# Kernel tuning notes

Measured on AMD Instinct MI355X. Metric: run time of the kernel, lower is better.

The kernel has to match this reference:

```python
import jax, jax.numpy as jnp
import numpy as np
from jax import lax

N_FRAMES = 256

def _conv(x, w, b):
    # NCHW conv, stride 3 on mel axis (matches MOSNet CNN that collapses mels 81->27->9->3->1)
    y = lax.conv_general_dilated(x, w, window_strides=(1, 3),
                                 padding=((1, 1), (1, 1)),
                                 dimension_numbers=('NCHW', 'OIHW', 'NCHW'))
    return jax.nn.relu(y + b[None, :, None, None])

def _lstm(x, Wih, Whh, bih, bhh, reverse=False):
    # x: [T, B, D] -> hs: [T, B, H]; PyTorch gate order i, f, g, o
    Bsz, H = x.shape[1], Whh.shape[1]
    bias = bih + bhh
    def step(carry, xt):
        h, c = carry
        z = xt @ Wih.T + h @ Whh.T + bias
        i, f, g, o = jnp.split(z, 4, axis=-1)
        c = jax.nn.sigmoid(f) * c + jax.nn.sigmoid(i) * jnp.tanh(g)
        h = jax.nn.sigmoid(o) * jnp.tanh(c)
        return (h, c), h
    init = (jnp.zeros((Bsz, H), x.dtype), jnp.zeros((Bsz, H), x.dtype))
    _, hs = lax.scan(step, init, x, reverse=reverse)
    return hs

def setup_inputs():
    key = jax.random.key(0)
    ks = jax.random.split(key, 24)
    B, T, M = 16, 4096, 81
    chans = [1, 16, 32, 64, 128]
    H = 128
    FC_IN = 2 * H * N_FRAMES  # 65536
    FC_H = 128
    s = 0.05
    inp = {'audio': jax.random.normal(ks[0], (B, T, M), jnp.float32),
           'sample_lengths': jnp.full((B,), T, dtype=jnp.int32)}
    for li in range(4):
        inp['w%d' % li] = jax.random.normal(ks[1 + 2 * li], (chans[li + 1], chans[li], 3, 3), jnp.float32) * s
        inp['b%d' % li] = jnp.zeros((chans[li + 1],), jnp.float32)
    D = chans[-1]
    for d, off in (('f', 9), ('b', 13)):
        inp['Wih_' + d] = jax.random.normal(ks[off], (4 * H, D), jnp.float32) * s
        inp['Whh_' + d] = jax.random.normal(ks[off + 1], (4 * H, H), jnp.float32) * s
        inp['bih_' + d] = jnp.zeros((4 * H,), jnp.float32)
        inp['bhh_' + d] = jnp.zeros((4 * H,), jnp.float32)
    inp['fc1_w'] = jax.random.normal(ks[17], (FC_H, FC_IN), jnp.float32) * 0.005
    inp['fc1_b'] = jnp.zeros((FC_H,), jnp.float32)
    inp['fs_w'] = jax.random.normal(ks[18], (1, FC_H), jnp.float32) * s
    inp['fs_b'] = jnp.zeros((1,), jnp.float32)
    return inp

def reference(audio, w0, b0, w1, b1, w2, b2, w3, b3,
              Wih_f, Whh_f, bih_f, bhh_f, Wih_b, Whh_b, bih_b, bhh_b,
              fc1_w, fc1_b, fs_w, fs_b, sample_lengths):
    B, T, M = audio.shape
    F = T // N_FRAMES  # all lengths == T, multiple of N_FRAMES -> all frames full
    x = audio.reshape(B * F, 1, N_FRAMES, M)   # [BF, 1, nf, mels]
    for w, b in ((w0, b0), (w1, b1), (w2, b2), (w3, b3)):
        x = _conv(x, w, b)                      # mel axis 81->27->9->3->1
    x = x[..., 0].transpose(2, 0, 1)            # [nf, BF, C]
    h_f = _lstm(x, Wih_f, Whh_f, bih_f, bhh_f)
    h_b = _lstm(x, Wih_b, Whh_b, bih_b, bhh_b, reverse=True)
    h = jnp.concatenate([h_f, h_b], axis=-1).transpose(1, 0, 2)  # [BF, nf, 2H]
    flat = h.reshape(B * F, -1)                 # time-major flatten, matches view(1,-1)
    z = jax.nn.relu(flat @ fc1_w.T + fc1_b)     # dropout is identity at inference
    score = jax.nn.sigmoid(z @ fs_w.T + fs_b) * 4.0 + 1.0  # mos range [1,5]
    frames = score.reshape(B, F)
    utt = frames.mean(axis=1)
    return utt, frames
```

## Files before the change

### kernel.cpp

```cpp
#include <hip/hip_runtime.h>
#include <hip/hip_fp16.h>

#define BF 256
#define TSTEPS 256

typedef _Float16 h8_t __attribute__((ext_vector_type(8)));
typedef _Float16 h4_t __attribute__((ext_vector_type(4)));
typedef float f4_t __attribute__((ext_vector_type(4)));

union H8 { uint4 u; h8_t v; };
union H4 { uint2 u; h4_t v; };
union U2H4 { uint2 u; __half h[4]; };

static __device__ __forceinline__ float sigmoidf_(float x) {
    return __builtin_amdgcn_rcpf(1.f + __expf(-x));
}
static __device__ __forceinline__ float tanhf_(float x) {
    return 1.f - 2.f * __builtin_amdgcn_rcpf(__expf(2.f * x) + 1.f);
}

static __device__ __forceinline__ void wg_barrier_lds() {
    __builtin_amdgcn_sched_barrier(0);
    asm volatile("s_waitcnt lgkmcnt(0)" ::: "memory");
    __builtin_amdgcn_s_barrier();
    __builtin_amdgcn_sched_barrier(0);
}

static __device__ __forceinline__ void pack_one(const float* __restrict__ src,
                                                __half* __restrict__ dst,
                                                int OC, int IC, int KS,
                                                int oc_str, int ic_str, int k_str, int i) {
    int grp = KS / 4;
    int j = i % grp;
    int oc = (i / grp) % OC;
    int g = (i / (grp * OC)) & 3;
    int chunk = i / (grp * OC * 4);
    int CPK = IC / KS;
    int cc = chunk % CPK;
    int khw = chunk / CPK;
    int ic = cc * KS + g * grp + j;
    dst[i] = __float2half(src[(long)oc * oc_str + (long)ic * ic_str + khw * k_str]);
}

static __device__ __forceinline__ void pack_whh_one(const float* __restrict__ src,
                                                    __half* __restrict__ dst, int i) {
    int j = i & 7;
    int prow = (i >> 3) & 511;
    int cg = i >> 12;
    int g = cg & 3, chunk = cg >> 2;
    int t = prow >> 4, rr = prow & 15;
    int cls = rr >> 2, du = rr & 3;
    int orig = cls * 128 + t * 4 + du;
    int ic = chunk * 32 + g * 8 + j;
    dst[i] = __float2half(src[orig * 128 + ic]);
}

__global__ __launch_bounds__(256) void prep_k(
        const float* __restrict__ w0, const float* __restrict__ w1,
        const float* __restrict__ w2, const float* __restrict__ w3,
        const float* __restrict__ Wihf, const float* __restrict__ Wihb,
        const float* __restrict__ Whhf, const float* __restrict__ Whhb,
        float* __restrict__ w0t, __half* __restrict__ w1p,
        __half* __restrict__ w2p, __half* __restrict__ w3p,
        __half* __restrict__ wfp, __half* __restrict__ wbp,
        __half* __restrict__ whhfp, __half* __restrict__ whhbp) {
    int i = blockIdx.x * 256 + threadIdx.x;
    if (i < 144) { int oc = i / 9, rem = i % 9; w0t[rem * 16 + oc] = w0[i]; return; }
    i -= 144;
    if (i < 4608) { pack_one(w1, w1p, 32, 16, 16, 144, 9, 1, i); return; }
    i -= 4608;
    if (i < 18432) { pack_one(w2, w2p, 64, 32, 32, 288, 9, 1, i); return; }
    i -= 18432;
    if (i < 73728) { pack_one(w3, w3p, 128, 64, 32, 576, 9, 1, i); return; }
    i -= 73728;
    if (i < 65536) { pack_one(Wihf, wfp, 512, 128, 32, 128, 1, 0, i); return; }
    i -= 65536;
    if (i < 65536) { pack_one(Wihb, wbp, 512, 128, 32, 128, 1, 0, i); return; }
    i -= 65536;
    if (i < 65536) { pack_whh_one(Whhf, whhfp, i); return; }
    i -= 65536;
    if (i < 65536) { pack_whh_one(Whhb, whhbp, i); return; }
}

__global__ void pack_wf16(const float* __restrict__ src, __half* __restrict__ dst,
                          int OC, int IC, int KS,
                          int oc_str, int ic_str, int k_str, int total) {
    int i = blockIdx.x * 256 + threadIdx.x;
    if (i >= total) return;
    pack_one(src, dst, OC, IC, KS, oc_str, ic_str, k_str, i);
}

__global__ __launch_bounds__(256) void conv0_k(const float* __restrict__ in,
                                               const float* __restrict__ wT,
                                               const float* __restrict__ bias,
                                               __half* __restrict__ out) {
    __shared__ float wsm[9][16];
    __shared__ float bs[16];
    int tid = threadIdx.x;
    if (tid < 144) wsm[tid / 16][tid % 16] = wT[tid];
    if (tid < 16) bs[tid] = bias[tid];
    __syncthreads();
    int gid = blockIdx.x * 256 + tid;
    int ow = gid % 27;
    int t = (gid / 27) % 256;
    int bf = gid / (27 * 256);
    float acc[16];
#pragma unroll
    for (int o = 0; o < 16; o++) acc[o] = bs[o];
    int iw0 = ow * 3 - 1;
#pragma unroll
    for (int kh = 0; kh < 3; kh++) {
        int tt = t + kh - 1;
        if ((unsigned)tt >= 256u) continue;
        const float* ip = in + ((long)bf * 256 + tt) * 81;
#pragma unroll
        for (int kw = 0; kw < 3; kw++) {
            int iw = iw0 + kw;
            if ((unsigned)iw >= 81u) continue;
            float x = ip[iw];
#pragma unroll
            for (int o = 0; o < 16; o++) acc[o] += x * wsm[kh * 3 + kw][o];
        }
    }
    __half2* op = (__half2*)(out + (long)gid * 16);
#pragma unroll
    for (int o = 0; o < 8; o++)
        op[o] = __floats2half2_rn(fmaxf(acc[2 * o], 0.f), fmaxf(acc[2 * o + 1], 0.f));
}

template<int IC, int OC, int WIN, int WOUT, int KS>
__global__ __launch_bounds__(256) void convM_k(const __half* __restrict__ in,
                                               const __half* __restrict__ wp,
                                               const float* __restrict__ bias,
                                               __half* __restrict__ out) {
    constexpr int NT = OC / 16;
    constexpr int CPK = IC / KS;
    constexpr int NCHUNK = 9 * CPK;
    constexpr int GRP = KS / 4;
    int tid = threadIdx.x;
    int lane = tid & 63;
    int wv = tid >> 6;
    int l15 = lane & 15;
    int g = lane >> 4;
    int m = blockIdx.x * 64 + wv * 16 + l15;
    int ow = m % WOUT;
    int t = (m / WOUT) % 256;
    int bf = m / (WOUT * 256);

    f4_t acc[NT];
#pragma unroll
    for (int nt = 0; nt < NT; nt++)
#pragma unroll
        for (int r = 0; r < 4; r++) acc[nt][r] = 0.f;

#pragma unroll
    for (int chunk = 0; chunk < NCHUNK; chunk++) {
        int khw = chunk / CPK, cc = chunk % CPK;
        int kh = khw / 3;
        int kw = khw - kh * 3;
        int tt = t + kh - 1;
        int iw = ow * 3 + kw - 1;
        bool ok = ((unsigned)tt < 256u) && ((unsigned)iw < (unsigned)WIN);
        long aoff = ok ? (((long)(bf * 256 + tt) * WIN + iw) * IC + cc * KS + g * GRP) : 0;
        if constexpr (KS == 32) {
            H8 af;
            af.u = *(const uint4*)(in + aoff);
            if (!ok) af.u = make_uint4(0u, 0u, 0u, 0u);
#pragma unroll
            for (int nt = 0; nt < NT; nt++) {
                H8 bf8;
                bf8.u = *(const uint4*)(wp + ((long)(chunk * 4 + g) * OC + nt * 16 + l15) * GRP);
                acc[nt] = __builtin_amdgcn_mfma_f32_16x16x32_f16(af.v, bf8.v, acc[nt], 0, 0, 0);
            }
        } else {
            H4 af;
            af.u = *(const uint2*)(in + aoff);
            if (!ok) af.u = make_uint2(0u, 0u);
#pragma unroll
            for (int nt = 0; nt < NT; nt++) {
                H4 bf4;
                bf4.u = *(const uint2*)(wp + ((long)(chunk * 4 + g) * OC + nt * 16 + l15) * GRP);
                acc[nt] = __builtin_amdgcn_mfma_f32_16x16x16f16(af.v, bf4.v, acc[nt], 0, 0, 0);
            }
        }
    }
    int orow = blockIdx.x * 64 + wv * 16 + g * 4;
#pragma unroll
    for (int nt = 0; nt < NT; nt++) {
        int oc = nt * 16 + l15;
        float b = bias[oc];
#pragma unroll
        for (int r = 0; r < 4; r++) {
            float v = fmaxf(acc[nt][r] + b, 0.f);
            out[(long)(orow + r) * OC + oc] = __float2half(v);
        }
    }
}

__global__ __launch_bounds__(256) void gates_k(const __half* __restrict__ X,
                                               const __half* __restrict__ wpf,
                                               const __half* __restrict__ wpb,
                                               const float* __restrict__ bf1,
                                               const float* __restrict__ bf2,
                                               const float* __restrict__ bb1,
                                               const float* __restrict__ bb2,
                                               __half* __restrict__ Gf,
                                               __half* __restrict__ Gb) {
    int dir = blockIdx.z;
    const __half* wp = dir ? wpb : wpf;
    const float* b1 = dir ? bb1 : bf1;
    const float* b2 = dir ? bb2 : bf2;
    __half* G = dir ? Gb : Gf;
    int tid = threadIdx.x;
    int lane = tid & 63;
    int wv = tid >> 6;
    int l15 = lane & 15;
    int g = lane >> 4;
    long r0 = (long)blockIdx.x * 128 + wv * 32;
    int n0 = blockIdx.y * 128;

    f4_t acc[2][8];
#pragma unroll
    for (int s = 0; s < 2; s++)
#pragma unroll
        for (int nt = 0; nt < 8; nt++)
#pragma unroll
            for (int r = 0; r < 4; r++) acc[s][nt][r] = 0.f;

#pragma unroll
    for (int chunk = 0; chunk < 4; chunk++) {
        H8 a0, a1;
        a0.u = *(const uint4*)(X + (r0 + l15) * 128 + chunk * 32 + g * 8);
        a1.u = *(const uint4*)(X + (r0 + 16 + l15) * 128 + chunk * 32 + g * 8);
#pragma unroll
        for (int nt = 0; nt < 8; nt++) {
            H8 bw;
            bw.u = *(const uint4*)(wp + ((long)(chunk * 4 + g) * 512 + n0 + nt * 16 + l15) * 8);
            acc[0][nt] = __builtin_amdgcn_mfma_f32_16x16x32_f16(a0.v, bw.v, acc[0][nt], 0, 0, 0);
            acc[1][nt] = __builtin_amdgcn_mfma_f32_16x16x32_f16(a1.v, bw.v, acc[1][nt], 0, 0, 0);
        }
    }
    int b = (int)(r0 >> 8);
#pragma unroll
    for (int nt = 0; nt < 8; nt++) {
        int col = n0 + nt * 16 + l15;
        float bias = b1[col] + b2[col];
        long base = ((long)b * 512 + col) * 256;
#pragma unroll
        for (int s = 0; s < 2; s++) {
            int tb = (int)(r0 & 255) + s * 16 + g * 4;
            U2H4 pk;
            if (!dir) {
#pragma unroll
                for (int r = 0; r < 4; r++) pk.h[r] = __float2half(acc[s][nt][r] + bias);
                *(uint2*)(G + base + tb) = pk.u;
            } else {
#pragma unroll
                for (int r = 0; r < 4; r++) pk.h[3 - r] = __float2half(acc[s][nt][r] + bias);
                *(uint2*)(G + base + (252 - tb)) = pk.u;
            }
        }
    }
}

__global__ __launch_bounds__(1024, 4) void lstm_k(const __half* __restrict__ Gf,
                                                  const __half* __restrict__ Gb,
                                                  const __half* __restrict__ whhfp,
                                                  const __half* __restrict__ whhbp,
                                                  __half* __restrict__ flat) {
    int bid = blockIdx.x;
    int dir = bid >> 7;
    int b0 = (bid & 127) * 2;
    const __half* G = dir ? Gb : Gf;
    const __half* wp = dir ? whhbp : whhfp;
    int tid = threadIdx.x;
    int w = tid >> 6;
    int lane = tid & 63;
    int l15 = lane & 15;
    int g2 = lane >> 4;
    int chn = l15 >> 3;
    int u8 = l15 & 7;
    int unit = w * 8 + u8;
    int tsel = (u8 >> 2) & 1;
    int du = u8 & 3;

    H8 afr[2][4];
#pragma unroll
    for (int t = 0; t < 2; t++) {
        int prow = (w * 2 + t) * 16 + l15;
#pragma unroll
        for (int c = 0; c < 4; c++)
            afr[t][c].u = *(const uint4*)(wp + ((long)((c * 4 + g2) * 512 + prow)) * 8);
    }

    __shared__ __align__(16) __half hbuf[2][2][128];
    if (tid < 256) hbuf[0][tid >> 7][tid & 127] = __float2half(0.f);
    __syncthreads();

    const __half* gb0 = G + (((long)(b0 + chn) * 512) + g2 * 128 + unit) * 256;

    float cst = 0.f;
    float ma = (g2 == 2) ? 2.f : 1.f;
    float mb = ma;
    float cb = (g2 == 2) ? -1.f : 0.f;
    const f4_t zero4 = {0.f, 0.f, 0.f, 0.f};

    H8 gc, gn;
    gc.u = *(const uint4*)(gb0);
    long fbase = (long)(b0 + chn) * 65536 + dir * 128 + unit;

    for (int to = 0; to < 32; to++) {
        if (to < 31) gn.u = *(const uint4*)(gb0 + (to + 1) * 8);
#pragma unroll
        for (int ti = 0; ti < 8; ti++) {
            int s = to * 8 + ti;
            int p = s & 1;
            H8 bfr[4];
#pragma unroll
            for (int c = 0; c < 4; c++)
                bfr[c].u = *(const uint4*)(&hbuf[p][chn][c * 32 + g2 * 8]);

            f4_t acc[2];
#pragma unroll
            for (int t = 0; t < 2; t++)
                acc[t] = __builtin_amdgcn_mfma_f32_16x16x32_f16(afr[t][0].v, bfr[0].v,
                                                                zero4, 0, 0, 0);
#pragma unroll
            for (int c = 1; c < 4; c++)
#pragma unroll
                for (int t = 0; t < 2; t++)
                    acc[t] = __builtin_amdgcn_mfma_f32_16x16x32_f16(afr[t][c].v, bfr[c].v,
                                                                    acc[t], 0, 0, 0);
            f4_t at;
#pragma unroll
            for (int e = 0; e < 4; e++) at[e] = tsel ? acc[1][e] : acc[0][e];
            float lo = (du & 1) ? at[1] : at[0];
            float hi = (du & 1) ? at[3] : at[2];
            float ev = (du & 2) ? hi : lo;

            float z = ev + (float)gc.v[ti];
            float a = sigmoidf_(ma * z) * mb + cb;

            float x1 = __shfl_xor(a, 32, 64);
            float pi = a * x1;
            float x2 = __shfl_xor(pi, 16, 64);
            float cn = a * cst + x2;
            cst = cn;
            float tc = tanhf_(cn);
            float x3 = __shfl_xor(tc, 32, 64);
            float h = a * x3;

            if (g2 == 3) {
                __half hh = __float2half(h);
                int ts = dir ? (255 - s) : s;
                hbuf[p ^ 1][chn][unit] = hh;
                flat[fbase + (long)ts * 256] = hh;
            }
            wg_barrier_lds();
        }
        gc = gn;
    }
}

__global__ __launch_bounds__(256) void fc1m_k(const __half* __restrict__ flat,
                                              const __half* __restrict__ wp,
                                              float* __restrict__ z) {
    int tid = threadIdx.x;
    int lane = tid & 63;
    int wv = tid >> 6;
    int l15 = lane & 15;
    int g = lane >> 4;
    int m0 = blockIdx.x * 64 + wv * 16;
    long k0 = (long)blockIdx.y * 1024;

    f4_t acc[8];
#pragma unroll
    for (int nt = 0; nt < 8; nt++)
#pragma unroll
        for (int r = 0; r < 4; r++) acc[nt][r] = 0.f;

    for (int c = 0; c < 32; c++) {
        long chunk = (k0 >> 5) + c;
        H8 af;
        af.u = *(const uint4*)(flat + (long)(m0 + l15) * 65536 + k0 + c * 32 + g * 8);
#pragma unroll
        for (int nt = 0; nt < 8; nt++) {
            H8 bw;
            bw.u = *(const uint4*)(wp + ((chunk * 4 + g) * 128 + nt * 16 + l15) * 8);
            acc[nt] = __builtin_amdgcn_mfma_f32_16x16x32_f16(af.v, bw.v, acc[nt], 0, 0, 0);
        }
    }
#pragma unroll
    for (int nt = 0; nt < 8; nt++)
#pragma unroll
        for (int r = 0; r < 4; r++)
            atomicAdd(&z[(m0 + g * 4 + r) * 128 + nt * 16 + l15], acc[nt][r]);
}

__global__ void zero_k(float* __restrict__ p, int n) {
    int i = blockIdx.x * 256 + threadIdx.x;
    if (i < n) p[i] = 0.f;
}

__global__ __launch_bounds__(256) void head_k(const float* __restrict__ z,
                                              const float* __restrict__ b1,
                                              const float* __restrict__ fsw,
                                              const float* __restrict__ fsb,
                                              float* __restrict__ out) {
    __shared__ float sf[256];
    int r = threadIdx.x;
    float acc = fsb[0];
#pragma unroll
    for (int j4 = 0; j4 < 32; j4++) {
        float4 zv = *(const float4*)&z[r * 128 + j4 * 4];
        float4 bv = *(const float4*)&b1[j4 * 4];
        float4 wv = *(const float4*)&fsw[j4 * 4];
        acc += fmaxf(zv.x + bv.x, 0.f) * wv.x;
        acc += fmaxf(zv.y + bv.y, 0.f) * wv.y;
        acc += fmaxf(zv.z + bv.z, 0.f) * wv.z;
        acc += fmaxf(zv.w + bv.w, 0.f) * wv.w;
    }
    float val = sigmoidf_(acc) * 4.f + 1.f;
    out[16 + r] = val;
    sf[r] = val;
    __syncthreads();
    if (r < 16) {
        float m = 0.f;
#pragma unroll
        for (int f = 0; f < 16; f++) m += sf[r * 16 + f];
        out[r] = m * (1.f / 16.f);
    }
}

extern "C" void kernel_launch(void* const* d_in, const int* in_sizes, int n_in,
                              void* d_out, int out_size, void* d_ws, size_t ws_size,
                              hipStream_t stream) {
    const float* audio = (const float*)d_in[0];
    const float* w0 = (const float*)d_in[2];
    const float* b0 = (const float*)d_in[3];
    const float* w1 = (const float*)d_in[4];
    const float* b1 = (const float*)d_in[5];
    const float* w2 = (const float*)d_in[6];
    const float* b2 = (const float*)d_in[7];
    const float* w3 = (const float*)d_in[8];
    const float* b3 = (const float*)d_in[9];
    const float* Wih_f = (const float*)d_in[10];
    const float* Whh_f = (const float*)d_in[11];
    const float* bih_f = (const float*)d_in[12];
    const float* bhh_f = (const float*)d_in[13];
    const float* Wih_b = (const float*)d_in[14];
    const float* Whh_b = (const float*)d_in[15];
    const float* bih_b = (const float*)d_in[16];
    const float* bhh_b = (const float*)d_in[17];
    const float* fc1_w = (const float*)d_in[18];
    const float* fc1_b = (const float*)d_in[19];
    const float* fs_w = (const float*)d_in[20];
    const float* fs_b = (const float*)d_in[21];
    float* out = (float*)d_out;

    char* ws = (char*)d_ws;
    __half* Gf    = (__half*)(ws);
    __half* out1  = (__half*)(ws);
    __half* fc1p  = (__half*)(ws);
    __half* Gb    = (__half*)(ws + 67108864);
    __half* flat16= (__half*)(ws + 134217728);
    __half* out0  = (__half*)(ws + 134217728);
    __half* X     = (__half*)(ws + 201326592);
    __half* out2  = (__half*)(ws + 218103808);
    char* rd = ws + 243269632;
    float*  w0t   = (float*)(rd);
    __half* w1p   = (__half*)(rd + 1024);
    __half* w2p   = (__half*)(rd + 10240);
    __half* w3p   = (__half*)(rd + 47104);
    __half* wfp   = (__half*)(rd + 194560);
    __half* wbp   = (__half*)(rd + 325632);
    __half* whhfp = (__half*)(rd + 456704);
    __half* whhbp = (__half*)(rd + 587776);
    float*  zbuf  = (float*)(rd + 718848);

    prep_k<<<1403, 256, 0, stream>>>(w0, w1, w2, w3, Wih_f, Wih_b, Whh_f, Whh_b,
                                     w0t, w1p, w2p, w3p, wfp, wbp, whhfp, whhbp);

    conv0_k<<<6912, 256, 0, stream>>>(audio, w0t, b0, out0);
    convM_k<16, 32, 27, 9, 16><<<9216, 256, 0, stream>>>(out0, w1p, b1, out1);
    convM_k<32, 64, 9, 3, 32><<<3072, 256, 0, stream>>>(out1, w2p, b2, out2);
    convM_k<64, 128, 3, 1, 32><<<1024, 256, 0, stream>>>(out2, w3p, b3, X);

    gates_k<<<dim3(512, 4, 2), 256, 0, stream>>>(X, wfp, wbp, bih_f, bhh_f,
                                                 bih_b, bhh_b, Gf, Gb);

    lstm_k<<<256, 1024, 0, stream>>>(Gf, Gb, whhfp, whhbp, flat16);

    pack_wf16<<<32768, 256, 0, stream>>>(fc1_w, fc1p, 128, 65536, 32, 65536, 1, 0, 8388608);
    zero_k<<<128, 256, 0, stream>>>(zbuf, 256 * 128);
    fc1m_k<<<dim3(4, 64), 256, 0, stream>>>(flat16, fc1p, zbuf);
    head_k<<<1, 256, 0, stream>>>(zbuf, fc1_b, fs_w, fs_b, out);
}
```

Before: 532.1 us.

## Give each LSTM workgroup one sequence with 512 threads instead of two

The recurrent LSTM kernel moves from 256 workgroups of 1024 threads, each handling two sequences, to 512 workgroups of 512 threads, each handling one sequence. Each wave now covers 16 hidden units with four MFMA tiles instead of eight units with two, and the Whh packing is remapped to match. The aim is shorter per-step barriers (fewer waves to synchronise) and more independent workgroups to spread across CUs. The cost is twice as many MFMAs per wave per step on the serial critical path and more register pressure from the larger weight fragments.

```diff
diff --git a/kernel.cpp b/kernel.cpp
--- a/kernel.cpp
+++ b/kernel.cpp
@@ -48,9 +48,10 @@
     int prow = (i >> 3) & 511;
     int cg = i >> 12;
     int g = cg & 3, chunk = cg >> 2;
-    int t = prow >> 4, rr = prow & 15;
+    int T = prow >> 4, rr = prow & 15;
     int cls = rr >> 2, du = rr & 3;
-    int orig = cls * 128 + t * 4 + du;
+    int unit = (T >> 2) * 16 + (T & 3) * 4 + du;
+    int orig = cls * 128 + unit;
     int ic = chunk * 32 + g * 8 + j;
     dst[i] = __float2half(src[orig * 128 + ic]);
 }
@@ -263,14 +264,14 @@
     }
 }
 
-__global__ __launch_bounds__(1024, 4) void lstm_k(const __half* __restrict__ Gf,
-                                                  const __half* __restrict__ Gb,
-                                                  const __half* __restrict__ whhfp,
-                                                  const __half* __restrict__ whhbp,
-                                                  __half* __restrict__ flat) {
+__global__ __launch_bounds__(512, 4) void lstm_k(const __half* __restrict__ Gf,
+                                                 const __half* __restrict__ Gb,
+                                                 const __half* __restrict__ whhfp,
+                                                 const __half* __restrict__ whhbp,
+                                                 __half* __restrict__ flat) {
     int bid = blockIdx.x;
-    int dir = bid >> 7;
-    int b0 = (bid & 127) * 2;
+    int dir = bid >> 8;
+    int seq = bid & 255;
     const __half* G = dir ? Gb : Gf;
     const __half* wp = dir ? whhbp : whhfp;
     int tid = threadIdx.x;
@@ -278,26 +279,24 @@
     int lane = tid & 63;
     int l15 = lane & 15;
     int g2 = lane >> 4;
-    int chn = l15 >> 3;
-    int u8 = l15 & 7;
-    int unit = w * 8 + u8;
-    int tsel = (u8 >> 2) & 1;
-    int du = u8 & 3;
-
-    H8 afr[2][4];
-#pragma unroll
-    for (int t = 0; t < 2; t++) {
-        int prow = (w * 2 + t) * 16 + l15;
+    int unit = w * 16 + l15;
+    int tsel = l15 >> 2;
+    int du = l15 & 3;
+
+    H8 afr[4][4];
+#pragma unroll
+    for (int t = 0; t < 4; t++) {
+        int prow = (w * 4 + t) * 16 + l15;
 #pragma unroll
         for (int c = 0; c < 4; c++)
             afr[t][c].u = *(const uint4*)(wp + ((long)((c * 4 + g2) * 512 + prow)) * 8);
     }
 
-    __shared__ __align__(16) __half hbuf[2][2][128];
-    if (tid < 256) hbuf[0][tid >> 7][tid & 127] = __float2half(0.f);
+    __shared__ __align__(16) __half hbuf[2][128];
+    if (tid < 64) ((unsigned int*)hbuf)[tid] = 0u;
     __syncthreads();
 
-    const __half* gb0 = G + (((long)(b0 + chn) * 512) + g2 * 128 + unit) * 256;
+    const __half* gb0 = G + (((long)seq * 512) + g2 * 128 + unit) * 256;
 
     float cst = 0.f;
     float ma = (g2 == 2) ? 2.f : 1.f;
@@ -307,7 +306,7 @@
 
     H8 gc, gn;
     gc.u = *(const uint4*)(gb0);
-    long fbase = (long)(b0 + chn) * 65536 + dir * 128 + unit;
+    long fbase = (long)seq * 65536 + dir * 128 + unit;
 
     for (int to = 0; to < 32; to++) {
         if (to < 31) gn.u = *(const uint4*)(gb0 + (to + 1) * 8);
@@ -318,25 +317,29 @@
             H8 bfr[4];
 #pragma unroll
             for (int c = 0; c < 4; c++)
-                bfr[c].u = *(const uint4*)(&hbuf[p][chn][c * 32 + g2 * 8]);
-
-            f4_t acc[2];
-#pragma unroll
-            for (int t = 0; t < 2; t++)
+                bfr[c].u = *(const uint4*)(&hbuf[p][c * 32 + g2 * 8]);
+
+            f4_t acc[4];
+#pragma unroll
+            for (int t = 0; t < 4; t++)
                 acc[t] = __builtin_amdgcn_mfma_f32_16x16x32_f16(afr[t][0].v, bfr[0].v,
                                                                 zero4, 0, 0, 0);
 #pragma unroll
             for (int c = 1; c < 4; c++)
 #pragma unroll
-                for (int t = 0; t < 2; t++)
+                for (int t = 0; t < 4; t++)
                     acc[t] = __builtin_amdgcn_mfma_f32_16x16x32_f16(afr[t][c].v, bfr[c].v,
                                                                     acc[t], 0, 0, 0);
-            f4_t at;
-#pragma unroll
-            for (int e = 0; e < 4; e++) at[e] = tsel ? acc[1][e] : acc[0][e];
-            float lo = (du & 1) ? at[1] : at[0];
-            float hi = (du & 1) ? at[3] : at[2];
-            float ev = (du & 2) ? hi : lo;
+            float evt[4];
+#pragma unroll
+            for (int t = 0; t < 4; t++) {
+                float lo = (du & 1) ? acc[t][1] : acc[t][0];
+                float hi = (du & 1) ? acc[t][3] : acc[t][2];
+                evt[t] = (du & 2) ? hi : lo;
+            }
+            float e01 = (tsel & 1) ? evt[1] : evt[0];
+            float e23 = (tsel & 1) ? evt[3] : evt[2];
+            float ev = (tsel & 2) ? e23 : e01;
 
             float z = ev + (float)gc.v[ti];
             float a = sigmoidf_(ma * z) * mb + cb;
@@ -353,7 +356,7 @@
             if (g2 == 3) {
                 __half hh = __float2half(h);
                 int ts = dir ? (255 - s) : s;
-                hbuf[p ^ 1][chn][unit] = hh;
+                hbuf[p ^ 1][unit] = hh;
                 flat[fbase + (long)ts * 256] = hh;
             }
             wg_barrier_lds();
@@ -489,7 +492,7 @@
     gates_k<<<dim3(512, 4, 2), 256, 0, stream>>>(X, wfp, wbp, bih_f, bhh_f,
                                                  bih_b, bhh_b, Gf, Gb);
 
-    lstm_k<<<256, 1024, 0, stream>>>(Gf, Gb, whhfp, whhbp, flat16);
+    lstm_k<<<512, 512, 0, stream>>>(Gf, Gb, whhfp, whhbp, flat16);
 
     pack_wf16<<<32768, 256, 0, stream>>>(fc1_w, fc1p, 128, 65536, 32, 65536, 1, 0, 8388608);
     zero_k<<<128, 256, 0, stream>>>(zbuf, 256 * 128);
```

New measurement: 597.1 us. 1.12x slower.
